# Kernel optimization log

Hardware: AMD Instinct MI355X
Metric: run time of the kernel (lower is better)

## Reference

```python
import jax, jax.numpy as jnp
import numpy as np

HID = 128  # args['hidden_size']


def preprocess_adj(A):
    # A: [B, N, N] -> D^{-1/2} (A + I) D^{-1/2}
    N = A.shape[1]
    A_hat = A + jnp.eye(N, dtype=A.dtype)
    d = jnp.sum(A_hat, axis=2)                     # [B, N]
    d_safe = jnp.where(d > 0, d, 1.0)
    d_inv = jnp.where(d > 0, d_safe ** -0.5, 0.0)  # inf -> 0, as in torch code
    return d_inv[:, :, None] * A_hat * d_inv[:, None, :]


def lstm(x, w_ih, w_hh, b_ih, b_hh):
    # x: [B, T, H]; PyTorch gate order i, f, g, o; zero init state
    B = x.shape[0]
    H = w_hh.shape[1]
    def step(carry, xt):
        h, c = carry
        z = xt @ w_ih.T + b_ih + h @ w_hh.T + b_hh
        i, f, g, o = jnp.split(z, 4, axis=-1)
        c = jax.nn.sigmoid(f) * c + jax.nn.sigmoid(i) * jnp.tanh(g)
        h = jax.nn.sigmoid(o) * jnp.tanh(c)
        return (h, c), h
    h0 = jnp.zeros((B, H), x.dtype)
    c0 = jnp.zeros((B, H), x.dtype)
    _, hs = jax.lax.scan(step, (h0, c0), jnp.swapaxes(x, 0, 1))
    return jnp.swapaxes(hs, 0, 1)  # [B, T, H]


def gcn_dynamic_forward(x, A_norm, conv_w, conv_b, w_ih, w_hh, b_ih, b_hh):
    # x: [B, N, HID] with N >= HID: take last HID rows as dynamic-filter input
    df_in = x[:, x.shape[1] - HID:, :]              # [B, HID, HID]
    dyn = jax.lax.conv_general_dilated(
        df_in, conv_w, window_strides=(1,), padding=[(1, 1)],
        dimension_numbers=('NCH', 'OIH', 'NCH')) + conv_b[None, :, None]
    lw = lstm(dyn, w_ih, w_hh, b_ih, b_hh)          # [B, HID, HID]
    agg = jnp.matmul(A_norm, x)                     # [B, N, HID]
    out = jax.nn.sigmoid(jnp.matmul(agg, lw))       # output activation (1-layer GCN)
    return out                                       # dropout is identity in eval


def setup_inputs() -> dict:
    key = jax.random.key(0)
    ks = jax.random.split(key, 8)
    B, N = 4, 4096
    node_embedding = jax.random.normal(ks[0], (B, N, HID), dtype=jnp.float32)
    # sparse symmetric-ish 0/1 adjacency, avg degree ~ N*0.01
    adjacency_matrix = (jax.random.uniform(ks[1], (B, N, N)) < 0.01).astype(jnp.float32)
    s = 0.05
    conv_w = jax.random.normal(ks[2], (HID, HID, 3), dtype=jnp.float32) * s
    conv_b = jax.random.normal(ks[3], (HID,), dtype=jnp.float32) * s
    w_ih = jax.random.normal(ks[4], (4 * HID, HID), dtype=jnp.float32) * s
    w_hh = jax.random.normal(ks[5], (4 * HID, HID), dtype=jnp.float32) * s
    b_ih = jax.random.normal(ks[6], (4 * HID,), dtype=jnp.float32) * s
    b_hh = jax.random.normal(ks[7], (4 * HID,), dtype=jnp.float32) * s
    return {"node_embedding": node_embedding, "adjacency_matrix": adjacency_matrix,
            "conv_w": conv_w, "conv_b": conv_b,
            "w_ih": w_ih, "w_hh": w_hh, "b_ih": b_ih, "b_hh": b_hh}


def reference(node_embedding, adjacency_matrix, conv_w, conv_b, w_ih, w_hh, b_ih, b_hh):
    A_norm = preprocess_adj(adjacency_matrix)
    return gcn_dynamic_forward(node_embedding, A_norm, conv_w, conv_b, w_ih, w_hh, b_ih, b_hh)
```

## Files before the change

kernel.cpp:

```cpp
#include <hip/hip_runtime.h>
#include <math.h>

#define N_NODES 4096
#define HIDN 128
#define MAXNZ 128

typedef float v4f __attribute__((ext_vector_type(4)));
typedef _Float16 h2 __attribute__((ext_vector_type(2)));
typedef _Float16 h8 __attribute__((ext_vector_type(8)));

__device__ __forceinline__ float fsig(float x) { return 1.0f / (1.0f + __expf(-x)); }
__device__ __forceinline__ float ftanh_(float x) { return 1.0f - 2.0f / (__expf(2.0f * x) + 1.0f); }

__global__ __launch_bounds__(512) void k_convz(
        const float* __restrict__ x, const float* __restrict__ conv_w,
        const float* __restrict__ conv_b, const float* __restrict__ w_ih,
        const float* __restrict__ b_ih, const float* __restrict__ b_hh,
        float* __restrict__ z3) {
    const int cb = blockIdx.x;
    const int b = cb >> 5;
    const int t0 = (cb & 31) * 4;
    const int tsub = threadIdx.x >> 7;
    const int h = threadIdx.x & 127;
    const int t = t0 + tsub;
    __shared__ __align__(16) float dyn_lds[4][HIDN];
    {
        const float* xb = x + ((size_t)b * N_NODES + (N_NODES - HIDN)) * HIDN;
        const float* w = conv_w + (size_t)t * HIDN * 3;
        float a0 = conv_b[t], a1 = 0.0f, a2 = 0.0f, a3 = 0.0f;
        #pragma unroll 4
        for (int i = 0; i < HIDN; i += 4) {
            const float* xr0 = xb + (size_t)i * HIDN;
            #pragma unroll
            for (int s = 0; s < 4; ++s) {
                const float* xr = xr0 + s * HIDN;
                float w0 = w[(i + s) * 3 + 0], w1 = w[(i + s) * 3 + 1], w2 = w[(i + s) * 3 + 2];
                float left  = (h > 0)   ? xr[h - 1] : 0.0f;
                float mid   = xr[h];
                float right = (h < 127) ? xr[h + 1] : 0.0f;
                if (s == 0)      a0 += left * w0 + mid * w1 + right * w2;
                else if (s == 1) a1 += left * w0 + mid * w1 + right * w2;
                else if (s == 2) a2 += left * w0 + mid * w1 + right * w2;
                else             a3 += left * w0 + mid * w1 + right * w2;
            }
        }
        dyn_lds[tsub][h] = (a0 + a1) + (a2 + a3);
    }
    __syncthreads();
    const int u = threadIdx.x;
    const int qg = u >> 7;
    const int m  = u & 127;
    const float4* wr = (const float4*)(w_ih + (size_t)u * HIDN);
    float bias = b_ih[u] + b_hh[u];
    float acc0 = bias, acc1 = bias, acc2 = bias, acc3 = bias;
    #pragma unroll
    for (int half = 0; half < 2; ++half) {
        float4 wv[16];
        #pragma unroll
        for (int j = 0; j < 16; ++j) wv[j] = wr[half * 16 + j];
        const float4* d0 = (const float4*)dyn_lds[0] + half * 16;
        const float4* d1 = (const float4*)dyn_lds[1] + half * 16;
        const float4* d2 = (const float4*)dyn_lds[2] + half * 16;
        const float4* d3 = (const float4*)dyn_lds[3] + half * 16;
        #pragma unroll
        for (int j = 0; j < 16; ++j) {
            float4 wj = wv[j];
            float4 v0 = d0[j], v1 = d1[j], v2 = d2[j], v3 = d3[j];
            acc0 += wj.x * v0.x + wj.y * v0.y + wj.z * v0.z + wj.w * v0.w;
            acc1 += wj.x * v1.x + wj.y * v1.y + wj.z * v1.z + wj.w * v1.w;
            acc2 += wj.x * v2.x + wj.y * v2.y + wj.z * v2.z + wj.w * v2.w;
            acc3 += wj.x * v3.x + wj.y * v3.y + wj.z * v3.z + wj.w * v3.w;
        }
    }
    float* zb = z3 + (size_t)b * HIDN * HIDN * 4;
    zb[((size_t)(t0 + 0) * 128 + m) * 4 + qg] = acc0;
    zb[((size_t)(t0 + 1) * 128 + m) * 4 + qg] = acc1;
    zb[((size_t)(t0 + 2) * 128 + m) * 4 + qg] = acc2;
    zb[((size_t)(t0 + 3) * 128 + m) * 4 + qg] = acc3;
}

__global__ __launch_bounds__(512, 2) void k_lstm_scan(
        const float* __restrict__ z3, const float* __restrict__ w_hh,
        float* __restrict__ lw,
        const float* __restrict__ A, float* __restrict__ d_inv,
        int* __restrict__ cnt, int* __restrict__ idx) {
    if (blockIdx.x < 4) {
        const int b = blockIdx.x;
        const int t = threadIdx.x;
        __shared__ __align__(16) h2 hbuf[2][64];
        __shared__ __align__(16) float4 zl[16 * 128];
        const int m = (t < 256) ? (t >> 1) : 0;
        const int half = t & 1;
        h2 w2[4][32];
        if (t < 256) {
            #pragma unroll
            for (int g = 0; g < 4; ++g) {
                const float4* wr = (const float4*)(w_hh + ((size_t)(g * HIDN + m)) * HIDN + half * 64);
                #pragma unroll
                for (int j4 = 0; j4 < 16; ++j4) {
                    float4 wv = wr[j4];
                    w2[g][2 * j4 + 0] = h2{(_Float16)wv.x, (_Float16)wv.y};
                    w2[g][2 * j4 + 1] = h2{(_Float16)wv.z, (_Float16)wv.w};
                }
            }
        }
        float c = 0.0f;
        if (t < 64) hbuf[0][t] = h2{(_Float16)0.0f, (_Float16)0.0f};
        const float4* zsrc = (const float4*)z3 + (size_t)b * 16384;
        for (int ch = 0; ch < 8; ++ch) {
            const float4* src = zsrc + ch * 2048;
            #pragma unroll
            for (int k = 0; k < 4; ++k)
                zl[t + 512 * k] = src[t + 512 * k];
            __syncthreads();
            if (t < 256) {
                float hist[16];
                #pragma unroll
                for (int si = 0; si < 16; ++si) {
                    const int s = ch * 16 + si;
                    const h8* hp = ((const h8*)hbuf[s & 1]) + half * 8;
                    h8 H0 = hp[0], H1 = hp[1], H2 = hp[2], H3 = hp[3];
                    h8 H4 = hp[4], H5 = hp[5], H6 = hp[6], H7 = hp[7];
                    h2 hh[32];
                    #pragma unroll
                    for (int j = 0; j < 4; ++j) {
                        hh[j]      = ((const h2*)&H0)[j];
                        hh[4 + j]  = ((const h2*)&H1)[j];
                        hh[8 + j]  = ((const h2*)&H2)[j];
                        hh[12 + j] = ((const h2*)&H3)[j];
                        hh[16 + j] = ((const h2*)&H4)[j];
                        hh[20 + j] = ((const h2*)&H5)[j];
                        hh[24 + j] = ((const h2*)&H6)[j];
                        hh[28 + j] = ((const h2*)&H7)[j];
                    }
                    float4 zv = zl[si * 128 + m];
                    float a0 = 0.f, b0 = 0.f, a1 = 0.f, b1 = 0.f;
                    float a2 = 0.f, b2 = 0.f, a3 = 0.f, b3 = 0.f;
                    #pragma unroll
                    for (int j = 0; j < 16; ++j) {
                        a0 = __builtin_amdgcn_fdot2(w2[0][2 * j], hh[2 * j], a0, false);
                        b0 = __builtin_amdgcn_fdot2(w2[0][2 * j + 1], hh[2 * j + 1], b0, false);
                        a1 = __builtin_amdgcn_fdot2(w2[1][2 * j], hh[2 * j], a1, false);
                        b1 = __builtin_amdgcn_fdot2(w2[1][2 * j + 1], hh[2 * j + 1], b1, false);
                        a2 = __builtin_amdgcn_fdot2(w2[2][2 * j], hh[2 * j], a2, false);
                        b2 = __builtin_amdgcn_fdot2(w2[2][2 * j + 1], hh[2 * j + 1], b2, false);
                        a3 = __builtin_amdgcn_fdot2(w2[3][2 * j], hh[2 * j], a3, false);
                        b3 = __builtin_amdgcn_fdot2(w2[3][2 * j + 1], hh[2 * j + 1], b3, false);
                    }
                    float p0 = a0 + b0, p1 = a1 + b1, p2 = a2 + b2, p3 = a3 + b3;
                    p0 += __shfl_xor(p0, 1);
                    p1 += __shfl_xor(p1, 1);
                    p2 += __shfl_xor(p2, 1);
                    p3 += __shfl_xor(p3, 1);
                    float zi = p0 + zv.x;
                    float zf = p1 + zv.y;
                    float zg = p2 + zv.z;
                    float zo = p3 + zv.w;
                    float ig = fsig(zi);
                    float fg = fsig(zf);
                    float gg = ftanh_(zg);
                    float og = fsig(zo);
                    c = fg * c + ig * gg;
                    float hn = og * ftanh_(c);
                    hist[si] = hn;
                    if (half == 0) ((_Float16*)hbuf[(s + 1) & 1])[m] = (_Float16)hn;
                    __syncthreads();
                }
                if (half == 0) {
                    float* lwb = lw + ((size_t)b * HIDN + ch * 16) * HIDN + m;
                    #pragma unroll
                    for (int si = 0; si < 16; ++si)
                        lwb[(size_t)si * HIDN] = hist[si];
                }
            } else {
                #pragma unroll
                for (int si = 0; si < 16; ++si) __syncthreads();
            }
        }
    } else {
        const int wid = threadIdx.x >> 6;
        const int lane = threadIdx.x & 63;
        const int r = (blockIdx.x - 4) * 8 + wid;
        const v4f* row = (const v4f*)(A + (size_t)r * N_NODES);
        __shared__ int sidx[8][MAXNZ];
        const unsigned long long below = (1ull << lane) - 1ull;
        int cbase = 0;
        v4f cur[4], nxt[4];
        #pragma unroll
        for (int j = 0; j < 4; ++j) cur[j] = row[j * 64 + lane];
#define PROC1(c, col)                                                         \
        {                                                                     \
            bool nz = ((c) != 0.0f);                                          \
            unsigned long long mm = __ballot(nz);                             \
            if (mm) {                                                         \
                if (nz) {                                                     \
                    int p_ = cbase + __popcll(mm & below);                    \
                    if (p_ < MAXNZ) sidx[wid][p_] = (col);                    \
                }                                                             \
                cbase += __popcll(mm);                                        \
            }                                                                 \
        }
        #pragma unroll
        for (int g = 0; g < 4; ++g) {
            if (g < 3) {
                #pragma unroll
                for (int j = 0; j < 4; ++j) nxt[j] = row[(g + 1) * 256 + j * 64 + lane];
            }
            #pragma unroll
            for (int j = 0; j < 4; ++j) {
                int col0 = ((g * 4 + j) * 64 + lane) * 4;
                PROC1(cur[j].x, col0 + 0);
                PROC1(cur[j].y, col0 + 1);
                PROC1(cur[j].z, col0 + 2);
                PROC1(cur[j].w, col0 + 3);
            }
            #pragma unroll
            for (int j = 0; j < 4; ++j) cur[j] = nxt[j];
        }
#undef PROC1
        int cnt_r = (cbase < MAXNZ) ? cbase : MAXNZ;
        for (int k = lane; k < cnt_r; k += 64)
            idx[r * MAXNZ + k] = sidx[wid][k];
        if (lane == 0) {
            cnt[r] = cnt_r;
            d_inv[r] = rsqrtf((float)(cbase + 1));
        }
    }
}

__global__ __launch_bounds__(512) void k_gather(
        const float* __restrict__ x, const float* __restrict__ d_inv,
        const int* __restrict__ cnt, const int* __restrict__ idx,
        float* __restrict__ agg) {
    const int gIdx = blockIdx.x;
    const int b = (gIdx & 7) >> 1;
    const int o = ((gIdx >> 3) << 1) | (gIdx & 1);
    const int wid = threadIdx.x >> 6;
    const int lane = threadIdx.x & 63;
    __shared__ __align__(16) float dl[N_NODES];
    {
        const float4* dsrc = (const float4*)(d_inv + (b << 12));
        float4* ddst = (float4*)dl;
        ddst[threadIdx.x] = dsrc[threadIdx.x];
        ddst[threadIdx.x + 512] = dsrc[threadIdx.x + 512];
    }
    __syncthreads();
    const int i = o * 8 + wid;
    const int r = (b << 12) + i;
    const float2* xb = (const float2*)(x + (size_t)b * N_NODES * HIDN);
    const int* irow = idx + r * MAXNZ;
    const int n = cnt[r];
    float ax = 0.0f, ay = 0.0f;
    int k = 0;
    for (; k + 8 <= n; k += 8) {
        int4 j0 = *(const int4*)&irow[k];
        int4 j1 = *(const int4*)&irow[k + 4];
        float2 v0 = xb[(size_t)j0.x * 64 + lane];
        float2 v1 = xb[(size_t)j0.y * 64 + lane];
        float2 v2 = xb[(size_t)j0.z * 64 + lane];
        float2 v3 = xb[(size_t)j0.w * 64 + lane];
        float2 v4 = xb[(size_t)j1.x * 64 + lane];
        float2 v5 = xb[(size_t)j1.y * 64 + lane];
        float2 v6 = xb[(size_t)j1.z * 64 + lane];
        float2 v7 = xb[(size_t)j1.w * 64 + lane];
        float d0 = dl[j0.x], d1 = dl[j0.y], d2 = dl[j0.z], d3 = dl[j0.w];
        float d4 = dl[j1.x], d5 = dl[j1.y], d6 = dl[j1.z], d7 = dl[j1.w];
        ax += d0 * v0.x + d1 * v1.x + d2 * v2.x + d3 * v3.x
            + d4 * v4.x + d5 * v5.x + d6 * v6.x + d7 * v7.x;
        ay += d0 * v0.y + d1 * v1.y + d2 * v2.y + d3 * v3.y
            + d4 * v4.y + d5 * v5.y + d6 * v6.y + d7 * v7.y;
    }
    for (; k < n; ++k) {
        int j = irow[k];
        float dj = dl[j];
        float2 v = xb[(size_t)j * 64 + lane];
        ax += dj * v.x;
        ay += dj * v.y;
    }
    float di = dl[i];
    float2 vi = xb[(size_t)i * 64 + lane];
    float2 o2;
    o2.x = di * (ax + di * vi.x);
    o2.y = di * (ay + di * vi.y);
    ((float2*)(agg + (size_t)r * HIDN))[lane] = o2;
}

__global__ __launch_bounds__(256) void k_outmm(
        const float* __restrict__ agg, const float* __restrict__ lw,
        float* __restrict__ out) {
    __shared__ __align__(16) float lw_lds[HIDN * HIDN];
    const int i0 = blockIdx.x * 64;
    const int b = i0 >> 12;
    const float4* lwg = (const float4*)(lw + (size_t)b * HIDN * HIDN);
    float4* lds4 = (float4*)lw_lds;
    for (int v = threadIdx.x; v < HIDN * HIDN / 4; v += 256) lds4[v] = lwg[v];
    __syncthreads();
    const int r0 = i0 + (threadIdx.x >> 3) * 2;
    const int u0 = (threadIdx.x & 7) * 16;
    const float4* a4 = (const float4*)agg;
    float4 acc[2][4];
    #pragma unroll
    for (int rr = 0; rr < 2; ++rr)
        #pragma unroll
        for (int cc = 0; cc < 4; ++cc) acc[rr][cc] = make_float4(0.f, 0.f, 0.f, 0.f);
    for (int f4 = 0; f4 < 32; ++f4) {
        float4 a0 = a4[(size_t)r0 * 32 + f4];
        float4 a1 = a4[(size_t)(r0 + 1) * 32 + f4];
        #pragma unroll
        for (int ff = 0; ff < 4; ++ff) {
            float af0 = (ff == 0) ? a0.x : (ff == 1) ? a0.y : (ff == 2) ? a0.z : a0.w;
            float af1 = (ff == 0) ? a1.x : (ff == 1) ? a1.y : (ff == 2) ? a1.z : a1.w;
            int f = f4 * 4 + ff;
            const float4* wrow = (const float4*)(lw_lds + f * HIDN + u0);
            #pragma unroll
            for (int cc = 0; cc < 4; ++cc) {
                float4 wv = wrow[cc];
                acc[0][cc].x += af0 * wv.x; acc[0][cc].y += af0 * wv.y;
                acc[0][cc].z += af0 * wv.z; acc[0][cc].w += af0 * wv.w;
                acc[1][cc].x += af1 * wv.x; acc[1][cc].y += af1 * wv.y;
                acc[1][cc].z += af1 * wv.z; acc[1][cc].w += af1 * wv.w;
            }
        }
    }
    #pragma unroll
    for (int rr = 0; rr < 2; ++rr) {
        #pragma unroll
        for (int cc = 0; cc < 4; ++cc) {
            float4 ov;
            ov.x = fsig(acc[rr][cc].x);
            ov.y = fsig(acc[rr][cc].y);
            ov.z = fsig(acc[rr][cc].z);
            ov.w = fsig(acc[rr][cc].w);
            *(float4*)(out + (size_t)(r0 + rr) * HIDN + u0 + cc * 4) = ov;
        }
    }
}

extern "C" void kernel_launch(void* const* d_in, const int* in_sizes, int n_in,
                              void* d_out, int out_size, void* d_ws, size_t ws_size,
                              hipStream_t stream) {
    const float* x      = (const float*)d_in[0];
    const float* A      = (const float*)d_in[1];
    const float* conv_w = (const float*)d_in[2];
    const float* conv_b = (const float*)d_in[3];
    const float* w_ih   = (const float*)d_in[4];
    const float* w_hh   = (const float*)d_in[5];
    const float* b_ih   = (const float*)d_in[6];
    const float* b_hh   = (const float*)d_in[7];
    float* out = (float*)d_out;

    char* ws = (char*)d_ws;
    float* d_inv = (float*)ws;
    int*   cnt   = (int*)(ws + 65536);
    int*   idx   = (int*)(ws + 131072);
    float* z3    = (float*)(ws + 131072 + 8388608);
    float* lw    = (float*)(ws + 131072 + 8388608 + 1048576);
    float* agg   = (float*)(ws + 131072 + 8388608 + 1048576 + 262144);

    hipLaunchKernelGGL(k_convz, dim3(128), dim3(512), 0, stream,
                       x, conv_w, conv_b, w_ih, b_ih, b_hh, z3);
    hipLaunchKernelGGL(k_lstm_scan, dim3(2052), dim3(512), 0, stream,
                       z3, w_hh, lw, A, d_inv, cnt, idx);
    hipLaunchKernelGGL(k_gather, dim3(2048), dim3(512), 0, stream,
                       x, d_inv, cnt, idx, agg);
    hipLaunchKernelGGL(k_outmm, dim3(256), dim3(256), 0, stream, agg, lw, out);
}
```

Baseline: 487.9 us.

## Regroup kernels to overlap LSTM scan with gather and split recurrence four ways

```diff
diff --git a/kernel.cpp b/kernel.cpp
--- a/kernel.cpp
+++ b/kernel.cpp
@@ -12,177 +12,80 @@
 __device__ __forceinline__ float fsig(float x) { return 1.0f / (1.0f + __expf(-x)); }
 __device__ __forceinline__ float ftanh_(float x) { return 1.0f - 2.0f / (__expf(2.0f * x) + 1.0f); }
 
-__global__ __launch_bounds__(512) void k_convz(
+__global__ __launch_bounds__(512) void k1_conv_ascan(
         const float* __restrict__ x, const float* __restrict__ conv_w,
         const float* __restrict__ conv_b, const float* __restrict__ w_ih,
         const float* __restrict__ b_ih, const float* __restrict__ b_hh,
-        float* __restrict__ z3) {
-    const int cb = blockIdx.x;
-    const int b = cb >> 5;
-    const int t0 = (cb & 31) * 4;
-    const int tsub = threadIdx.x >> 7;
-    const int h = threadIdx.x & 127;
-    const int t = t0 + tsub;
-    __shared__ __align__(16) float dyn_lds[4][HIDN];
-    {
-        const float* xb = x + ((size_t)b * N_NODES + (N_NODES - HIDN)) * HIDN;
-        const float* w = conv_w + (size_t)t * HIDN * 3;
-        float a0 = conv_b[t], a1 = 0.0f, a2 = 0.0f, a3 = 0.0f;
-        #pragma unroll 4
-        for (int i = 0; i < HIDN; i += 4) {
-            const float* xr0 = xb + (size_t)i * HIDN;
-            #pragma unroll
-            for (int s = 0; s < 4; ++s) {
-                const float* xr = xr0 + s * HIDN;
-                float w0 = w[(i + s) * 3 + 0], w1 = w[(i + s) * 3 + 1], w2 = w[(i + s) * 3 + 2];
-                float left  = (h > 0)   ? xr[h - 1] : 0.0f;
-                float mid   = xr[h];
-                float right = (h < 127) ? xr[h + 1] : 0.0f;
-                if (s == 0)      a0 += left * w0 + mid * w1 + right * w2;
-                else if (s == 1) a1 += left * w0 + mid * w1 + right * w2;
-                else if (s == 2) a2 += left * w0 + mid * w1 + right * w2;
-                else             a3 += left * w0 + mid * w1 + right * w2;
-            }
-        }
-        dyn_lds[tsub][h] = (a0 + a1) + (a2 + a3);
-    }
-    __syncthreads();
-    const int u = threadIdx.x;
-    const int qg = u >> 7;
-    const int m  = u & 127;
-    const float4* wr = (const float4*)(w_ih + (size_t)u * HIDN);
-    float bias = b_ih[u] + b_hh[u];
-    float acc0 = bias, acc1 = bias, acc2 = bias, acc3 = bias;
-    #pragma unroll
-    for (int half = 0; half < 2; ++half) {
-        float4 wv[16];
-        #pragma unroll
-        for (int j = 0; j < 16; ++j) wv[j] = wr[half * 16 + j];
-        const float4* d0 = (const float4*)dyn_lds[0] + half * 16;
-        const float4* d1 = (const float4*)dyn_lds[1] + half * 16;
-        const float4* d2 = (const float4*)dyn_lds[2] + half * 16;
-        const float4* d3 = (const float4*)dyn_lds[3] + half * 16;
-        #pragma unroll
-        for (int j = 0; j < 16; ++j) {
-            float4 wj = wv[j];
-            float4 v0 = d0[j], v1 = d1[j], v2 = d2[j], v3 = d3[j];
-            acc0 += wj.x * v0.x + wj.y * v0.y + wj.z * v0.z + wj.w * v0.w;
-            acc1 += wj.x * v1.x + wj.y * v1.y + wj.z * v1.z + wj.w * v1.w;
-            acc2 += wj.x * v2.x + wj.y * v2.y + wj.z * v2.z + wj.w * v2.w;
-            acc3 += wj.x * v3.x + wj.y * v3.y + wj.z * v3.z + wj.w * v3.w;
-        }
-    }
-    float* zb = z3 + (size_t)b * HIDN * HIDN * 4;
-    zb[((size_t)(t0 + 0) * 128 + m) * 4 + qg] = acc0;
-    zb[((size_t)(t0 + 1) * 128 + m) * 4 + qg] = acc1;
-    zb[((size_t)(t0 + 2) * 128 + m) * 4 + qg] = acc2;
-    zb[((size_t)(t0 + 3) * 128 + m) * 4 + qg] = acc3;
-}
-
-__global__ __launch_bounds__(512, 2) void k_lstm_scan(
-        const float* __restrict__ z3, const float* __restrict__ w_hh,
-        float* __restrict__ lw,
+        float* __restrict__ z3,
         const float* __restrict__ A, float* __restrict__ d_inv,
         int* __restrict__ cnt, int* __restrict__ idx) {
-    if (blockIdx.x < 4) {
-        const int b = blockIdx.x;
-        const int t = threadIdx.x;
-        __shared__ __align__(16) h2 hbuf[2][64];
-        __shared__ __align__(16) float4 zl[16 * 128];
-        const int m = (t < 256) ? (t >> 1) : 0;
-        const int half = t & 1;
-        h2 w2[4][32];
-        if (t < 256) {
-            #pragma unroll
-            for (int g = 0; g < 4; ++g) {
-                const float4* wr = (const float4*)(w_hh + ((size_t)(g * HIDN + m)) * HIDN + half * 64);
+    __shared__ __align__(16) float dyn_lds[4][HIDN];
+    __shared__ int sidx[8][MAXNZ];
+    if (blockIdx.x < 128) {
+        const int cb = blockIdx.x;
+        const int b = cb >> 5;
+        const int t0 = (cb & 31) * 4;
+        const int tsub = threadIdx.x >> 7;
+        const int h = threadIdx.x & 127;
+        const int t = t0 + tsub;
+        {
+            const float* xb = x + ((size_t)b * N_NODES + (N_NODES - HIDN)) * HIDN;
+            const float* w = conv_w + (size_t)t * HIDN * 3;
+            float a0 = conv_b[t], a1 = 0.0f, a2 = 0.0f, a3 = 0.0f;
+            #pragma unroll 4
+            for (int i = 0; i < HIDN; i += 4) {
+                const float* xr0 = xb + (size_t)i * HIDN;
                 #pragma unroll
-                for (int j4 = 0; j4 < 16; ++j4) {
-                    float4 wv = wr[j4];
-                    w2[g][2 * j4 + 0] = h2{(_Float16)wv.x, (_Float16)wv.y};
-                    w2[g][2 * j4 + 1] = h2{(_Float16)wv.z, (_Float16)wv.w};
+                for (int s = 0; s < 4; ++s) {
+                    const float* xr = xr0 + s * HIDN;
+                    float w0 = w[(i + s) * 3 + 0], w1 = w[(i + s) * 3 + 1], w2 = w[(i + s) * 3 + 2];
+                    float left  = (h > 0)   ? xr[h - 1] : 0.0f;
+                    float mid   = xr[h];
+                    float right = (h < 127) ? xr[h + 1] : 0.0f;
+                    if (s == 0)      a0 += left * w0 + mid * w1 + right * w2;
+                    else if (s == 1) a1 += left * w0 + mid * w1 + right * w2;
+                    else if (s == 2) a2 += left * w0 + mid * w1 + right * w2;
+                    else             a3 += left * w0 + mid * w1 + right * w2;
                 }
             }
-        }
-        float c = 0.0f;
-        if (t < 64) hbuf[0][t] = h2{(_Float16)0.0f, (_Float16)0.0f};
-        const float4* zsrc = (const float4*)z3 + (size_t)b * 16384;
-        for (int ch = 0; ch < 8; ++ch) {
-            const float4* src = zsrc + ch * 2048;
-            #pragma unroll
-            for (int k = 0; k < 4; ++k)
-                zl[t + 512 * k] = src[t + 512 * k];
-            __syncthreads();
-            if (t < 256) {
-                float hist[16];
-                #pragma unroll
-                for (int si = 0; si < 16; ++si) {
-                    const int s = ch * 16 + si;
-                    const h8* hp = ((const h8*)hbuf[s & 1]) + half * 8;
-                    h8 H0 = hp[0], H1 = hp[1], H2 = hp[2], H3 = hp[3];
-                    h8 H4 = hp[4], H5 = hp[5], H6 = hp[6], H7 = hp[7];
-                    h2 hh[32];
-                    #pragma unroll
-                    for (int j = 0; j < 4; ++j) {
-                        hh[j]      = ((const h2*)&H0)[j];
-                        hh[4 + j]  = ((const h2*)&H1)[j];
-                        hh[8 + j]  = ((const h2*)&H2)[j];
-                        hh[12 + j] = ((const h2*)&H3)[j];
-                        hh[16 + j] = ((const h2*)&H4)[j];
-                        hh[20 + j] = ((const h2*)&H5)[j];
-                        hh[24 + j] = ((const h2*)&H6)[j];
-                        hh[28 + j] = ((const h2*)&H7)[j];
-                    }
-                    float4 zv = zl[si * 128 + m];
-                    float a0 = 0.f, b0 = 0.f, a1 = 0.f, b1 = 0.f;
-                    float a2 = 0.f, b2 = 0.f, a3 = 0.f, b3 = 0.f;
-                    #pragma unroll
-                    for (int j = 0; j < 16; ++j) {
-                        a0 = __builtin_amdgcn_fdot2(w2[0][2 * j], hh[2 * j], a0, false);
-                        b0 = __builtin_amdgcn_fdot2(w2[0][2 * j + 1], hh[2 * j + 1], b0, false);
-                        a1 = __builtin_amdgcn_fdot2(w2[1][2 * j], hh[2 * j], a1, false);
-                        b1 = __builtin_amdgcn_fdot2(w2[1][2 * j + 1], hh[2 * j + 1], b1, false);
-                        a2 = __builtin_amdgcn_fdot2(w2[2][2 * j], hh[2 * j], a2, false);
-                        b2 = __builtin_amdgcn_fdot2(w2[2][2 * j + 1], hh[2 * j + 1], b2, false);
-                        a3 = __builtin_amdgcn_fdot2(w2[3][2 * j], hh[2 * j], a3, false);
-                        b3 = __builtin_amdgcn_fdot2(w2[3][2 * j + 1], hh[2 * j + 1], b3, false);
-                    }
-                    float p0 = a0 + b0, p1 = a1 + b1, p2 = a2 + b2, p3 = a3 + b3;
-                    p0 += __shfl_xor(p0, 1);
-                    p1 += __shfl_xor(p1, 1);
-                    p2 += __shfl_xor(p2, 1);
-                    p3 += __shfl_xor(p3, 1);
-                    float zi = p0 + zv.x;
-                    float zf = p1 + zv.y;
-                    float zg = p2 + zv.z;
-                    float zo = p3 + zv.w;
-                    float ig = fsig(zi);
-                    float fg = fsig(zf);
-                    float gg = ftanh_(zg);
-                    float og = fsig(zo);
-                    c = fg * c + ig * gg;
-                    float hn = og * ftanh_(c);
-                    hist[si] = hn;
-                    if (half == 0) ((_Float16*)hbuf[(s + 1) & 1])[m] = (_Float16)hn;
-                    __syncthreads();
-                }
-                if (half == 0) {
-                    float* lwb = lw + ((size_t)b * HIDN + ch * 16) * HIDN + m;
-                    #pragma unroll
-                    for (int si = 0; si < 16; ++si)
-                        lwb[(size_t)si * HIDN] = hist[si];
-                }
-            } else {
-                #pragma unroll
-                for (int si = 0; si < 16; ++si) __syncthreads();
-            }
-        }
+            dyn_lds[tsub][h] = (a0 + a1) + (a2 + a3);
+        }
+        __syncthreads();
+        const int u = threadIdx.x;
+        const int qg = u >> 7;
+        const int m  = u & 127;
+        const float4* wr = (const float4*)(w_ih + (size_t)u * HIDN);
+        float bias = b_ih[u] + b_hh[u];
+        float acc0 = bias, acc1 = bias, acc2 = bias, acc3 = bias;
+        #pragma unroll
+        for (int half = 0; half < 2; ++half) {
+            float4 wv[16];
+            #pragma unroll
+            for (int j = 0; j < 16; ++j) wv[j] = wr[half * 16 + j];
+            const float4* d0 = (const float4*)dyn_lds[0] + half * 16;
+            const float4* d1 = (const float4*)dyn_lds[1] + half * 16;
+            const float4* d2 = (const float4*)dyn_lds[2] + half * 16;
+            const float4* d3 = (const float4*)dyn_lds[3] + half * 16;
+            #pragma unroll
+            for (int j = 0; j < 16; ++j) {
+                float4 wj = wv[j];
+                float4 v0 = d0[j], v1 = d1[j], v2 = d2[j], v3 = d3[j];
+                acc0 += wj.x * v0.x + wj.y * v0.y + wj.z * v0.z + wj.w * v0.w;
+                acc1 += wj.x * v1.x + wj.y * v1.y + wj.z * v1.z + wj.w * v1.w;
+                acc2 += wj.x * v2.x + wj.y * v2.y + wj.z * v2.z + wj.w * v2.w;
+                acc3 += wj.x * v3.x + wj.y * v3.y + wj.z * v3.z + wj.w * v3.w;
+            }
+        }
+        float* zb = z3 + (size_t)b * HIDN * HIDN * 4;
+        zb[((size_t)(t0 + 0) * 128 + m) * 4 + qg] = acc0;
+        zb[((size_t)(t0 + 1) * 128 + m) * 4 + qg] = acc1;
+        zb[((size_t)(t0 + 2) * 128 + m) * 4 + qg] = acc2;
+        zb[((size_t)(t0 + 3) * 128 + m) * 4 + qg] = acc3;
     } else {
         const int wid = threadIdx.x >> 6;
         const int lane = threadIdx.x & 63;
-        const int r = (blockIdx.x - 4) * 8 + wid;
+        const int r = (blockIdx.x - 128) * 8 + wid;
         const v4f* row = (const v4f*)(A + (size_t)r * N_NODES);
-        __shared__ int sidx[8][MAXNZ];
         const unsigned long long below = (1ull << lane) - 1ull;
         int cbase = 0;
         v4f cur[4], nxt[4];
@@ -228,61 +131,138 @@
     }
 }
 
-__global__ __launch_bounds__(512) void k_gather(
+__global__ __launch_bounds__(512, 2) void k2_lstm_gather(
+        const float* __restrict__ z3, const float* __restrict__ w_hh,
+        float* __restrict__ lw,
         const float* __restrict__ x, const float* __restrict__ d_inv,
         const int* __restrict__ cnt, const int* __restrict__ idx,
         float* __restrict__ agg) {
-    const int gIdx = blockIdx.x;
-    const int b = (gIdx & 7) >> 1;
-    const int o = ((gIdx >> 3) << 1) | (gIdx & 1);
-    const int wid = threadIdx.x >> 6;
-    const int lane = threadIdx.x & 63;
-    __shared__ __align__(16) float dl[N_NODES];
-    {
-        const float4* dsrc = (const float4*)(d_inv + (b << 12));
-        float4* ddst = (float4*)dl;
-        ddst[threadIdx.x] = dsrc[threadIdx.x];
-        ddst[threadIdx.x + 512] = dsrc[threadIdx.x + 512];
+    __shared__ __align__(16) float4 zl[16 * 128];
+    __shared__ __align__(16) _Float16 hbuf[2][HIDN];
+    if (blockIdx.x < 4) {
+        const int b = blockIdx.x;
+        const int t = threadIdx.x;
+        const int m = t >> 2;
+        const int q = t & 3;
+        h2 w2[4][16];
+        #pragma unroll
+        for (int g = 0; g < 4; ++g) {
+            const float4* wr = (const float4*)(w_hh + ((size_t)(g * HIDN + m)) * HIDN + q * 32);
+            #pragma unroll
+            for (int j4 = 0; j4 < 8; ++j4) {
+                float4 wv = wr[j4];
+                w2[g][2 * j4 + 0] = h2{(_Float16)wv.x, (_Float16)wv.y};
+                w2[g][2 * j4 + 1] = h2{(_Float16)wv.z, (_Float16)wv.w};
+            }
+        }
+        float c = 0.0f;
+        if (t < 64) ((h2*)hbuf[0])[t] = h2{(_Float16)0.0f, (_Float16)0.0f};
+        const float4* zsrc = (const float4*)z3 + (size_t)b * 16384;
+        float* lwb = lw + (size_t)b * HIDN * HIDN + m;
+        float hist[4];
+        for (int ch = 0; ch < 8; ++ch) {
+            const float4* src = zsrc + ch * 2048;
+            #pragma unroll
+            for (int k = 0; k < 4; ++k)
+                zl[t + 512 * k] = src[t + 512 * k];
+            __syncthreads();
+            #pragma unroll
+            for (int si = 0; si < 16; ++si) {
+                const int s = ch * 16 + si;
+                const h8* hp = ((const h8*)hbuf[s & 1]) + q * 4;
+                h8 H0 = hp[0], H1 = hp[1], H2 = hp[2], H3 = hp[3];
+                h2 hh[16];
+                #pragma unroll
+                for (int j = 0; j < 4; ++j) {
+                    hh[j]      = ((const h2*)&H0)[j];
+                    hh[4 + j]  = ((const h2*)&H1)[j];
+                    hh[8 + j]  = ((const h2*)&H2)[j];
+                    hh[12 + j] = ((const h2*)&H3)[j];
+                }
+                float4 zv = zl[si * 128 + m];
+                float a0 = 0.f, a1 = 0.f, a2 = 0.f, a3 = 0.f;
+                #pragma unroll
+                for (int j = 0; j < 16; ++j) {
+                    a0 = __builtin_amdgcn_fdot2(w2[0][j], hh[j], a0, false);
+                    a1 = __builtin_amdgcn_fdot2(w2[1][j], hh[j], a1, false);
+                    a2 = __builtin_amdgcn_fdot2(w2[2][j], hh[j], a2, false);
+                    a3 = __builtin_amdgcn_fdot2(w2[3][j], hh[j], a3, false);
+                }
+                a0 += __shfl_xor(a0, 1); a0 += __shfl_xor(a0, 2);
+                a1 += __shfl_xor(a1, 1); a1 += __shfl_xor(a1, 2);
+                a2 += __shfl_xor(a2, 1); a2 += __shfl_xor(a2, 2);
+                a3 += __shfl_xor(a3, 1); a3 += __shfl_xor(a3, 2);
+                float zi = a0 + zv.x;
+                float zf = a1 + zv.y;
+                float zg = a2 + zv.z;
+                float zo = a3 + zv.w;
+                float ig = fsig(zi);
+                float fg = fsig(zf);
+                float gg = ftanh_(zg);
+                float og = fsig(zo);
+                c = fg * c + ig * gg;
+                float hn = og * ftanh_(c);
+                if (q == (si & 3)) hist[si >> 2] = hn;
+                if (q == 0) hbuf[(s + 1) & 1][m] = (_Float16)hn;
+                __syncthreads();
+            }
+            #pragma unroll
+            for (int j = 0; j < 4; ++j)
+                lwb[(size_t)(ch * 16 + q + 4 * j) * HIDN] = hist[j];
+        }
+    } else {
+        const int gIdx = blockIdx.x - 4;
+        const int b = (gIdx & 7) >> 1;
+        const int o = ((gIdx >> 3) << 1) | (gIdx & 1);
+        const int wid = threadIdx.x >> 6;
+        const int lane = threadIdx.x & 63;
+        float* dl = (float*)zl;
+        {
+            const float4* dsrc = (const float4*)(d_inv + (b << 12));
+            float4* ddst = (float4*)dl;
+            ddst[threadIdx.x] = dsrc[threadIdx.x];
+            ddst[threadIdx.x + 512] = dsrc[threadIdx.x + 512];
+        }
+        __syncthreads();
+        const int i = o * 8 + wid;
+        const int r = (b << 12) + i;
+        const float2* xb = (const float2*)(x + (size_t)b * N_NODES * HIDN);
+        const int* irow = idx + r * MAXNZ;
+        const int n = cnt[r];
+        float ax = 0.0f, ay = 0.0f;
+        int k = 0;
+        for (; k + 8 <= n; k += 8) {
+            int4 j0 = *(const int4*)&irow[k];
+            int4 j1 = *(const int4*)&irow[k + 4];
+            float2 v0 = xb[(size_t)j0.x * 64 + lane];
+            float2 v1 = xb[(size_t)j0.y * 64 + lane];
+            float2 v2 = xb[(size_t)j0.z * 64 + lane];
+            float2 v3 = xb[(size_t)j0.w * 64 + lane];
+            float2 v4 = xb[(size_t)j1.x * 64 + lane];
+            float2 v5 = xb[(size_t)j1.y * 64 + lane];
+            float2 v6 = xb[(size_t)j1.z * 64 + lane];
+            float2 v7 = xb[(size_t)j1.w * 64 + lane];
+            float d0 = dl[j0.x], d1 = dl[j0.y], d2 = dl[j0.z], d3 = dl[j0.w];
+            float d4 = dl[j1.x], d5 = dl[j1.y], d6 = dl[j1.z], d7 = dl[j1.w];
+            ax += d0 * v0.x + d1 * v1.x + d2 * v2.x + d3 * v3.x
+                + d4 * v4.x + d5 * v5.x + d6 * v6.x + d7 * v7.x;
+            ay += d0 * v0.y + d1 * v1.y + d2 * v2.y + d3 * v3.y
+                + d4 * v4.y + d5 * v5.y + d6 * v6.y + d7 * v7.y;
+        }
+        for (; k < n; ++k) {
+            int j = irow[k];
+            float dj = dl[j];
+            float2 v = xb[(size_t)j * 64 + lane];
+            ax += dj * v.x;
+            ay += dj * v.y;
+        }
+        float di = dl[i];
+        float2 vi = xb[(size_t)i * 64 + lane];
+        float2 o2;
+        o2.x = di * (ax + di * vi.x);
+        o2.y = di * (ay + di * vi.y);
+        ((float2*)(agg + (size_t)r * HIDN))[lane] = o2;
     }
-    __syncthreads();
-    const int i = o * 8 + wid;
-    const int r = (b << 12) + i;
-    const float2* xb = (const float2*)(x + (size_t)b * N_NODES * HIDN);
-    const int* irow = idx + r * MAXNZ;
-    const int n = cnt[r];
-    float ax = 0.0f, ay = 0.0f;
-    int k = 0;
-    for (; k + 8 <= n; k += 8) {
-        int4 j0 = *(const int4*)&irow[k];
-        int4 j1 = *(const int4*)&irow[k + 4];
-        float2 v0 = xb[(size_t)j0.x * 64 + lane];
-        float2 v1 = xb[(size_t)j0.y * 64 + lane];
-        float2 v2 = xb[(size_t)j0.z * 64 + lane];
-        float2 v3 = xb[(size_t)j0.w * 64 + lane];
-        float2 v4 = xb[(size_t)j1.x * 64 + lane];
-        float2 v5 = xb[(size_t)j1.y * 64 + lane];
-        float2 v6 = xb[(size_t)j1.z * 64 + lane];
-        float2 v7 = xb[(size_t)j1.w * 64 + lane];
-        float d0 = dl[j0.x], d1 = dl[j0.y], d2 = dl[j0.z], d3 = dl[j0.w];
-        float d4 = dl[j1.x], d5 = dl[j1.y], d6 = dl[j1.z], d7 = dl[j1.w];
-        ax += d0 * v0.x + d1 * v1.x + d2 * v2.x + d3 * v3.x
-            + d4 * v4.x + d5 * v5.x + d6 * v6.x + d7 * v7.x;
-        ay += d0 * v0.y + d1 * v1.y + d2 * v2.y + d3 * v3.y
-            + d4 * v4.y + d5 * v5.y + d6 * v6.y + d7 * v7.y;
-    }
-    for (; k < n; ++k) {
-        int j = irow[k];
-        float dj = dl[j];
-        float2 v = xb[(size_t)j * 64 + lane];
-        ax += dj * v.x;
-        ay += dj * v.y;
-    }
-    float di = dl[i];
-    float2 vi = xb[(size_t)i * 64 + lane];
-    float2 o2;
-    o2.x = di * (ax + di * vi.x);
-    o2.y = di * (ay + di * vi.y);
-    ((float2*)(agg + (size_t)r * HIDN))[lane] = o2;
 }
 
 __global__ __launch_bounds__(256) void k_outmm(
@@ -357,11 +337,9 @@
     float* lw    = (float*)(ws + 131072 + 8388608 + 1048576);
     float* agg   = (float*)(ws + 131072 + 8388608 + 1048576 + 262144);
 
-    hipLaunchKernelGGL(k_convz, dim3(128), dim3(512), 0, stream,
-                       x, conv_w, conv_b, w_ih, b_ih, b_hh, z3);
-    hipLaunchKernelGGL(k_lstm_scan, dim3(2052), dim3(512), 0, stream,
-                       z3, w_hh, lw, A, d_inv, cnt, idx);
-    hipLaunchKernelGGL(k_gather, dim3(2048), dim3(512), 0, stream,
-                       x, d_inv, cnt, idx, agg);
+    hipLaunchKernelGGL(k1_conv_ascan, dim3(2176), dim3(512), 0, stream,
+                       x, conv_w, conv_b, w_ih, b_ih, b_hh, z3, A, d_inv, cnt, idx);
+    hipLaunchKernelGGL(k2_lstm_gather, dim3(2052), dim3(512), 0, stream,
+                       z3, w_hh, lw, x, d_inv, cnt, idx, agg);
     hipLaunchKernelGGL(k_outmm, dim3(256), dim3(256), 0, stream, agg, lw, out);
 }
```

Measured after the change: 500.7 us. +2.6%, slower.
